# Optimization experiments

Hardware: AMD Instinct MI355X
Metric: run time of the kernel (lower is better)

## Reference

```python
import jax, jax.numpy as jnp
import numpy as np

D_MODEL, D_FF, N_EXP, TOP_K = 1024, 2048, 8, 2


def _silu(x):
    return x * jax.nn.sigmoid(x)


def setup_inputs() -> dict:
    key = jax.random.key(0)
    ks = jax.random.split(key, 8)
    s_d = 1.0 / np.sqrt(D_MODEL)
    s_f = 1.0 / np.sqrt(D_FF)
    x = jax.random.normal(ks[0], (2, 2048, D_MODEL), dtype=jnp.float32)
    Wr = jax.random.normal(ks[1], (D_MODEL, N_EXP), dtype=jnp.float32) * s_d
    W1 = jax.random.normal(ks[2], (N_EXP, D_MODEL, D_FF), dtype=jnp.float32) * s_d
    W2 = jax.random.normal(ks[3], (N_EXP, D_FF, D_MODEL), dtype=jnp.float32) * s_f
    W3 = jax.random.normal(ks[4], (N_EXP, D_MODEL, D_FF), dtype=jnp.float32) * s_d
    Ws1 = jax.random.normal(ks[5], (D_MODEL, D_FF), dtype=jnp.float32) * s_d
    Ws2 = jax.random.normal(ks[6], (D_FF, D_MODEL), dtype=jnp.float32) * s_f
    Ws3 = jax.random.normal(ks[7], (D_MODEL, D_FF), dtype=jnp.float32) * s_d
    return {"x": x, "Wr": Wr, "W1": W1, "W2": W2, "W3": W3,
            "Ws1": Ws1, "Ws2": Ws2, "Ws3": Ws3}


def reference(x, Wr, W1, W2, W3, Ws1, Ws2, Ws3):
    B, S, D = x.shape
    T = B * S
    # router
    logits = jnp.einsum('bsd,de->bse', x, Wr)                     # [B,S,E]
    z_loss = jnp.mean(jax.nn.logsumexp(logits, axis=-1) ** 2)
    router_probs = jax.nn.softmax(logits, axis=-1)
    topk_logits, topk_idx = jax.lax.top_k(logits, TOP_K)          # [B,S,K]
    topk_gates = jax.nn.softmax(topk_logits, axis=-1)             # top_k > 1 branch
    # load-balance loss
    p = jnp.mean(router_probs, axis=(0, 1))                       # [E]
    dispatch = jax.nn.one_hot(topk_idx, N_EXP, dtype=router_probs.dtype)  # [B,S,K,E]
    f = jnp.mean(dispatch, axis=(0, 1, 2))                        # [E]
    lb_loss = N_EXP * jnp.sum(p * f)
    # expert compute: run all experts densely, then gather routed outputs
    xf = x.reshape(T, D)
    h = _silu(jnp.einsum('td,edf->etf', xf, W1)) * jnp.einsum('td,edf->etf', xf, W3)
    y = jnp.einsum('etf,efd->etd', h, W2)                         # [E,T,D]
    yt = jnp.transpose(y, (1, 0, 2))                              # [T,E,D]
    idx_flat = topk_idx.reshape(T, TOP_K)
    gates_flat = topk_gates.reshape(T, TOP_K)
    sel = jnp.take_along_axis(yt, idx_flat[:, :, None], axis=1)   # [T,K,D]
    out_flat = jnp.sum(gates_flat[:, :, None] * sel, axis=1)      # [T,D]
    tokens_per_expert = jnp.sum(dispatch.reshape(-1, N_EXP), axis=0) / (T * TOP_K)
    # shared expert (applied sequentially; 1 shared expert here)
    out = out_flat.reshape(B, S, D)
    out = jnp.einsum('bsf,fd->bsd', _silu(jnp.einsum('bsd,df->bsf', out, Ws1)) * jnp.einsum('bsd,df->bsf', out, Ws3), Ws2)
    return (out, tokens_per_expert, z_loss, z_loss * 0.001, lb_loss, lb_loss * 0.1)
```

## Files before the change

### kernel.cpp

```cpp
#include <hip/hip_runtime.h>

#define TOKENS 4096
#define DM 1024
#define DFF 2048
#define NE 8
#define CAP 2048

typedef unsigned short u16;
typedef __attribute__((ext_vector_type(8))) __bf16 bf16x8;
typedef __attribute__((ext_vector_type(8))) unsigned short u16x8;
typedef __attribute__((ext_vector_type(4))) float f32x4;

#define GL16(g, l)                                                                        \
  __builtin_amdgcn_global_load_lds((const __attribute__((address_space(1))) void*)(g),    \
                                   (__attribute__((address_space(3))) void*)(l), 16, 0, 0)

__device__ __forceinline__ u16 f2bf(float f) {
  unsigned int u = __builtin_bit_cast(unsigned int, f);
  unsigned int r = (u + 0x7FFFu + ((u >> 16) & 1u)) >> 16;
  return (u16)r;
}
__device__ __forceinline__ float bf2f(u16 h) {
  unsigned int u = ((unsigned int)h) << 16;
  return __builtin_bit_cast(float, u);
}

__global__ void zero_k(int* counters) {
  if (threadIdx.x < NE) counters[threadIdx.x] = 0;
}

__global__ void conv_k(const float* __restrict__ src, u16* __restrict__ dst, int n4) {
  int i = blockIdx.x * 256 + threadIdx.x;
  if (i >= n4) return;
  float4 v = ((const float4*)src)[i];
  ushort4 ov = make_ushort4(f2bf(v.x), f2bf(v.y), f2bf(v.z), f2bf(v.w));
  ((ushort4*)dst)[i] = ov;
}

__global__ void tconv_k(const float* __restrict__ src, u16* __restrict__ dst, int K, int N) {
  __shared__ u16 tile[64][68];
  const int k0 = blockIdx.x * 64;
  const int n0 = blockIdx.y * 64;
  const size_t zoff = (size_t)blockIdx.z * K * N;
  const float* s = src + zoff;
  u16* d = dst + zoff;
  const int tid = threadIdx.x;
#pragma unroll
  for (int p = 0; p < 4; ++p) {
    int idx = p * 256 + tid;
    int kr = idx >> 4;
    int nc = (idx & 15) * 4;
    float4 v = *(const float4*)(s + (size_t)(k0 + kr) * N + (n0 + nc));
    tile[kr][nc + 0] = f2bf(v.x);
    tile[kr][nc + 1] = f2bf(v.y);
    tile[kr][nc + 2] = f2bf(v.z);
    tile[kr][nc + 3] = f2bf(v.w);
  }
  __syncthreads();
#pragma unroll
  for (int p = 0; p < 4; ++p) {
    int idx = p * 256 + tid;
    int nr = idx >> 4;
    int kc = (idx & 15) * 4;
    ushort4 ov = make_ushort4(tile[kc + 0][nr], tile[kc + 1][nr], tile[kc + 2][nr], tile[kc + 3][nr]);
    *(ushort4*)(d + (size_t)(n0 + nr) * K + (k0 + kc)) = ov;
  }
}

__global__ void router_k(const float* __restrict__ x, const float* __restrict__ Wr,
                         int* __restrict__ counters, int* __restrict__ tok_list,
                         int* __restrict__ tok_e, int* __restrict__ tok_slot,
                         float* __restrict__ tok_gate, float* __restrict__ tok_probs,
                         float* __restrict__ tok_lse) {
  const int t = blockIdx.x;
  const int l = threadIdx.x;
  float acc[NE];
#pragma unroll
  for (int e = 0; e < NE; ++e) acc[e] = 0.f;
  const float* xr = x + (size_t)t * DM;
#pragma unroll
  for (int it = 0; it < DM / 64; ++it) {
    int d = it * 64 + l;
    float xv = xr[d];
    const float4* wr = (const float4*)(Wr + (size_t)d * NE);
    float4 w0 = wr[0], w1 = wr[1];
    acc[0] += xv * w0.x; acc[1] += xv * w0.y; acc[2] += xv * w0.z; acc[3] += xv * w0.w;
    acc[4] += xv * w1.x; acc[5] += xv * w1.y; acc[6] += xv * w1.z; acc[7] += xv * w1.w;
  }
#pragma unroll
  for (int off = 32; off >= 1; off >>= 1) {
#pragma unroll
    for (int e = 0; e < NE; ++e) acc[e] += __shfl_xor(acc[e], off, 64);
  }
  if (l == 0) {
    float m = acc[0];
#pragma unroll
    for (int e = 1; e < NE; ++e) m = fmaxf(m, acc[e]);
    float ex[NE], s = 0.f;
#pragma unroll
    for (int e = 0; e < NE; ++e) { ex[e] = expf(acc[e] - m); s += ex[e]; }
    float inv = 1.f / s;
#pragma unroll
    for (int e = 0; e < NE; ++e) tok_probs[t * NE + e] = ex[e] * inv;
    tok_lse[t] = m + logf(s);
    int i0 = 0; float l0 = acc[0];
#pragma unroll
    for (int e = 1; e < NE; ++e) if (acc[e] > l0) { l0 = acc[e]; i0 = e; }
    int i1 = -1; float l1 = -3.0e38f;
#pragma unroll
    for (int e = 0; e < NE; ++e) if (e != i0 && acc[e] > l1) { l1 = acc[e]; i1 = e; }
    float e1 = expf(l1 - l0);
    float g0 = 1.f / (1.f + e1);
    float g1 = e1 / (1.f + e1);
    int p0 = atomicAdd(&counters[i0], 1);
    int p1 = atomicAdd(&counters[i1], 1);
    if (p0 < CAP) tok_list[i0 * CAP + p0] = t;
    if (p1 < CAP) tok_list[i1 * CAP + p1] = t;
    tok_e[t * 2 + 0] = i0; tok_e[t * 2 + 1] = i1;
    tok_slot[t * 2 + 0] = p0; tok_slot[t * 2 + 1] = p1;
    tok_gate[t * 2 + 0] = g0; tok_gate[t * 2 + 1] = g1;
  }
}

__global__ void finalize_k(const float* __restrict__ tok_probs, const float* __restrict__ tok_lse,
                           const int* __restrict__ counters, float* __restrict__ tail) {
  __shared__ float s_p[NE];
  __shared__ float s_z;
  const int tid = threadIdx.x;
  if (tid == 0) s_z = 0.f;
  if (tid < NE) s_p[tid] = 0.f;
  __syncthreads();
  float lp[NE] = {0, 0, 0, 0, 0, 0, 0, 0};
  float lz = 0.f;
  for (int t = tid; t < TOKENS; t += 256) {
    float l = tok_lse[t];
    lz += l * l;
#pragma unroll
    for (int e = 0; e < NE; ++e) lp[e] += tok_probs[t * NE + e];
  }
#pragma unroll
  for (int off = 32; off >= 1; off >>= 1) {
    lz += __shfl_xor(lz, off, 64);
#pragma unroll
    for (int e = 0; e < NE; ++e) lp[e] += __shfl_xor(lp[e], off, 64);
  }
  if ((tid & 63) == 0) {
    atomicAdd(&s_z, lz);
    for (int e = 0; e < NE; ++e) atomicAdd(&s_p[e], lp[e]);
  }
  __syncthreads();
  if (tid == 0) {
    float z = s_z / (float)TOKENS;
    float lb = 0.f;
    for (int e = 0; e < NE; ++e) {
      float f = (float)counters[e] / (float)(TOKENS * 2);
      float p = s_p[e] / (float)TOKENS;
      lb += p * f;
      tail[e] = f;
    }
    lb *= (float)NE;
    tail[8] = z;
    tail[9] = z * 0.001f;
    tail[10] = lb;
    tail[11] = lb * 0.1f;
  }
}

__launch_bounds__(256, 2)
__global__ void gemm1_k(const u16* __restrict__ A, const u16* __restrict__ B1g,
                        const u16* __restrict__ B3g, u16* __restrict__ Hout,
                        const int* __restrict__ tok_list, const int* __restrict__ counts,
                        int Mfix) {
  constexpr int K = DM;
  constexpr int N = DFF;
  const int e = blockIdx.z;
  int n_e = counts ? counts[e] : Mfix;
  if (counts && n_e > CAP) n_e = CAP;
  const int m_base = blockIdx.x * 128;
  if (m_base >= n_e) return;
  const int n_base = blockIdx.y * 128;
  const size_t bstride = counts ? (size_t)N * K : 0;
  const u16* B1 = B1g + (size_t)e * bstride;
  const u16* B3 = B3g + (size_t)e * bstride;

  __shared__ __align__(16) u16 Als[128 * 32];
  __shared__ __align__(16) u16 B1ls[128 * 32];
  __shared__ __align__(16) u16 B3ls[128 * 32];

  const int tid = threadIdx.x;
  const int lane = tid & 63;
  const int w = tid >> 6;
  const int wm = w >> 1, wn = w & 1;
  const int lo = lane & 15, hi = lane >> 4;

  const int c0 = 2 * w;
  const int r0 = c0 * 16 + (lane >> 2);
  const int r1 = r0 + 16;
  const int sg = lane & 3;

  size_t ar0, ar1;
  if (tok_list) {
    int g0i = m_base + r0; if (g0i >= n_e) g0i = n_e - 1;
    int g1i = m_base + r1; if (g1i >= n_e) g1i = n_e - 1;
    ar0 = (size_t)tok_list[e * CAP + g0i];
    ar1 = (size_t)tok_list[e * CAP + g1i];
  } else {
    ar0 = (size_t)(m_base + r0);
    ar1 = (size_t)(m_base + r1);
  }
  const u16* pA0 = A + ar0 * (size_t)K + sg * 8;
  const u16* pA1 = A + ar1 * (size_t)K + sg * 8;
  const u16* pB1a = B1 + (size_t)(n_base + r0) * K + sg * 8;
  const u16* pB1b = B1 + (size_t)(n_base + r1) * K + sg * 8;
  const u16* pB3a = B3 + (size_t)(n_base + r0) * K + sg * 8;
  const u16* pB3b = B3 + (size_t)(n_base + r1) * K + sg * 8;
  u16* lA0 = &Als[c0 * 512];  u16* lA1 = &Als[c0 * 512 + 512];
  u16* lB1a = &B1ls[c0 * 512]; u16* lB1b = &B1ls[c0 * 512 + 512];
  u16* lB3a = &B3ls[c0 * 512]; u16* lB3b = &B3ls[c0 * 512 + 512];

  f32x4 acc1[4][4], acc3[4][4];
#pragma unroll
  for (int i = 0; i < 4; ++i)
#pragma unroll
    for (int j = 0; j < 4; ++j) { acc1[i][j] = (f32x4)0.f; acc3[i][j] = (f32x4)0.f; }

  for (int kt = 0; kt < K / 32; ++kt) {
    __syncthreads();
    const int ko = kt * 32;
    GL16(pA0 + ko, lA0);
    GL16(pA1 + ko, lA1);
    GL16(pB1a + ko, lB1a);
    GL16(pB1b + ko, lB1b);
    GL16(pB3a + ko, lB3a);
    GL16(pB3b + ko, lB3b);
    __syncthreads();
    bf16x8 af[4], b1f[4], b3f[4];
#pragma unroll
    for (int i = 0; i < 4; ++i) {
      af[i] = *(const bf16x8*)&Als[(wm * 64 + i * 16 + lo) * 32 + hi * 8];
      b1f[i] = *(const bf16x8*)&B1ls[(wn * 64 + i * 16 + lo) * 32 + hi * 8];
      b3f[i] = *(const bf16x8*)&B3ls[(wn * 64 + i * 16 + lo) * 32 + hi * 8];
    }
#pragma unroll
    for (int i = 0; i < 4; ++i)
#pragma unroll
      for (int j = 0; j < 4; ++j) {
        acc1[i][j] = __builtin_amdgcn_mfma_f32_16x16x32_bf16(af[i], b1f[j], acc1[i][j], 0, 0, 0);
        acc3[i][j] = __builtin_amdgcn_mfma_f32_16x16x32_bf16(af[i], b3f[j], acc3[i][j], 0, 0, 0);
      }
  }

  const size_t orow0 = (counts ? (size_t)e * CAP : 0) + m_base;
#pragma unroll
  for (int i = 0; i < 4; ++i) {
#pragma unroll
    for (int r = 0; r < 4; ++r) {
      int rl = wm * 64 + i * 16 + hi * 4 + r;
      if (m_base + rl < n_e) {
        u16* orow = Hout + (orow0 + rl) * (size_t)N + n_base;
#pragma unroll
        for (int j = 0; j < 4; ++j) {
          float s1 = acc1[i][j][r], s3 = acc3[i][j][r];
          float hv = s1 / (1.f + __expf(-s1)) * s3;
          orow[wn * 64 + j * 16 + lo] = f2bf(hv);
        }
      }
    }
  }
}

__launch_bounds__(256, 2)
__global__ void gemm2_k(const u16* __restrict__ Ag, const u16* __restrict__ Bg,
                        void* __restrict__ Outv, const int* __restrict__ counts, int Mfix,
                        int outFloat) {
  constexpr int K = DFF;
  constexpr int N = DM;
  const int e = blockIdx.z;
  int n_e = counts ? counts[e] : Mfix;
  if (counts && n_e > CAP) n_e = CAP;
  const int m_base = blockIdx.x * 128;
  if (m_base >= n_e) return;
  const int n_base = blockIdx.y * 128;
  const u16* A = Ag + (counts ? (size_t)e * CAP * K : 0);
  const u16* B = Bg + (counts ? (size_t)e * N * K : 0);

  __shared__ __align__(16) u16 Als[128 * 32];
  __shared__ __align__(16) u16 Bls[128 * 32];

  const int tid = threadIdx.x;
  const int lane = tid & 63;
  const int w = tid >> 6;
  const int wm = w >> 1, wn = w & 1;
  const int lo = lane & 15, hi = lane >> 4;

  const int c0 = 2 * w;
  const int r0 = c0 * 16 + (lane >> 2);
  const int r1 = r0 + 16;
  const int sg = lane & 3;

  const u16* pA0 = A + (size_t)(m_base + r0) * K + sg * 8;
  const u16* pA1 = A + (size_t)(m_base + r1) * K + sg * 8;
  const u16* pB0 = B + (size_t)(n_base + r0) * K + sg * 8;
  const u16* pB1 = B + (size_t)(n_base + r1) * K + sg * 8;
  u16* lA0 = &Als[c0 * 512]; u16* lA1 = &Als[c0 * 512 + 512];
  u16* lB0 = &Bls[c0 * 512]; u16* lB1 = &Bls[c0 * 512 + 512];

  f32x4 acc[4][4];
#pragma unroll
  for (int i = 0; i < 4; ++i)
#pragma unroll
    for (int j = 0; j < 4; ++j) acc[i][j] = (f32x4)0.f;

  for (int kt = 0; kt < K / 32; ++kt) {
    __syncthreads();
    const int ko = kt * 32;
    GL16(pA0 + ko, lA0);
    GL16(pA1 + ko, lA1);
    GL16(pB0 + ko, lB0);
    GL16(pB1 + ko, lB1);
    __syncthreads();
    bf16x8 af[4], bfg[4];
#pragma unroll
    for (int i = 0; i < 4; ++i) {
      af[i] = *(const bf16x8*)&Als[(wm * 64 + i * 16 + lo) * 32 + hi * 8];
      bfg[i] = *(const bf16x8*)&Bls[(wn * 64 + i * 16 + lo) * 32 + hi * 8];
    }
#pragma unroll
    for (int i = 0; i < 4; ++i)
#pragma unroll
      for (int j = 0; j < 4; ++j)
        acc[i][j] = __builtin_amdgcn_mfma_f32_16x16x32_bf16(af[i], bfg[j], acc[i][j], 0, 0, 0);
  }

#pragma unroll
  for (int i = 0; i < 4; ++i) {
#pragma unroll
    for (int r = 0; r < 4; ++r) {
      int rl = wm * 64 + i * 16 + hi * 4 + r;
      if (m_base + rl < n_e) {
        if (outFloat) {
          float* orow = (float*)Outv + (size_t)(m_base + rl) * N + n_base;
#pragma unroll
          for (int j = 0; j < 4; ++j) orow[wn * 64 + j * 16 + lo] = acc[i][j][r];
        } else {
          u16* orow = (u16*)Outv + ((size_t)e * CAP + m_base + rl) * N + n_base;
#pragma unroll
          for (int j = 0; j < 4; ++j) orow[wn * 64 + j * 16 + lo] = f2bf(acc[i][j][r]);
        }
      }
    }
  }
}

__global__ void combine_k(const u16* __restrict__ Y, const int* __restrict__ tok_e,
                          const int* __restrict__ tok_slot, const float* __restrict__ tok_gate,
                          u16* __restrict__ xs) {
  int u = blockIdx.x * 256 + threadIdx.x;
  int t = u >> 7;
  int seg = (u & 127) * 8;
  int e0 = tok_e[t * 2 + 0], e1 = tok_e[t * 2 + 1];
  int s0 = tok_slot[t * 2 + 0], s1 = tok_slot[t * 2 + 1];
  float g0 = tok_gate[t * 2 + 0], g1 = tok_gate[t * 2 + 1];
  u16x8 y0 = *(const u16x8*)(Y + ((size_t)e0 * CAP + s0) * DM + seg);
  u16x8 y1 = *(const u16x8*)(Y + ((size_t)e1 * CAP + s1) * DM + seg);
  u16x8 o;
#pragma unroll
  for (int j = 0; j < 8; ++j) o[j] = f2bf(g0 * bf2f(y0[j]) + g1 * bf2f(y1[j]));
  *(u16x8*)(xs + (size_t)t * DM + seg) = o;
}

extern "C" void kernel_launch(void* const* d_in, const int* in_sizes, int n_in, void* d_out,
                              int out_size, void* d_ws, size_t ws_size, hipStream_t stream) {
  const float* x = (const float*)d_in[0];
  const float* Wr = (const float*)d_in[1];
  const float* W1 = (const float*)d_in[2];
  const float* W2 = (const float*)d_in[3];
  const float* W3 = (const float*)d_in[4];
  const float* Ws1 = (const float*)d_in[5];
  const float* Ws2 = (const float*)d_in[6];
  const float* Ws3 = (const float*)d_in[7];
  float* out = (float*)d_out;
  (void)in_sizes; (void)n_in; (void)out_size; (void)ws_size;

  char* ws = (char*)d_ws;
  size_t o = 0;
  auto alloc = [&](size_t b) {
    void* p = ws + o;
    o = (o + b + 255) & ~(size_t)255;
    return p;
  };
  int* counters = (int*)alloc(NE * 4);
  int* tok_e = (int*)alloc(TOKENS * 2 * 4);
  int* tok_slot = (int*)alloc(TOKENS * 2 * 4);
  float* tok_gate = (float*)alloc(TOKENS * 2 * 4);
  float* tok_probs = (float*)alloc(TOKENS * NE * 4);
  float* tok_lse = (float*)alloc(TOKENS * 4);
  int* tok_list = (int*)alloc(NE * CAP * 4);
  u16* xb = (u16*)alloc((size_t)TOKENS * DM * 2);
  u16* W1t = (u16*)alloc((size_t)NE * DFF * DM * 2);
  u16* W3t = (u16*)alloc((size_t)NE * DFF * DM * 2);
  u16* W2t = (u16*)alloc((size_t)NE * DM * DFF * 2);
  u16* Ws1t = (u16*)alloc((size_t)DFF * DM * 2);
  u16* Ws3t = (u16*)alloc((size_t)DFF * DM * 2);
  u16* Ws2t = (u16*)alloc((size_t)DM * DFF * 2);
  u16* H = (u16*)alloc((size_t)NE * CAP * DFF * 2);
  u16* Y = (u16*)alloc((size_t)NE * CAP * DM * 2);
  u16* xs = (u16*)alloc((size_t)TOKENS * DM * 2);
  u16* Hs = (u16*)alloc((size_t)TOKENS * DFF * 2);

  zero_k<<<1, 64, 0, stream>>>(counters);
  conv_k<<<TOKENS * DM / 4 / 256, 256, 0, stream>>>(x, xb, TOKENS * DM / 4);
  tconv_k<<<dim3(DM / 64, DFF / 64, NE), 256, 0, stream>>>(W1, W1t, DM, DFF);
  tconv_k<<<dim3(DM / 64, DFF / 64, NE), 256, 0, stream>>>(W3, W3t, DM, DFF);
  tconv_k<<<dim3(DFF / 64, DM / 64, NE), 256, 0, stream>>>(W2, W2t, DFF, DM);
  tconv_k<<<dim3(DM / 64, DFF / 64, 1), 256, 0, stream>>>(Ws1, Ws1t, DM, DFF);
  tconv_k<<<dim3(DM / 64, DFF / 64, 1), 256, 0, stream>>>(Ws3, Ws3t, DM, DFF);
  tconv_k<<<dim3(DFF / 64, DM / 64, 1), 256, 0, stream>>>(Ws2, Ws2t, DFF, DM);
  router_k<<<TOKENS, 64, 0, stream>>>(x, Wr, counters, tok_list, tok_e, tok_slot, tok_gate,
                                      tok_probs, tok_lse);
  finalize_k<<<1, 256, 0, stream>>>(tok_probs, tok_lse, counters, out + (size_t)TOKENS * DM);
  gemm1_k<<<dim3(CAP / 128, DFF / 128, NE), 256, 0, stream>>>(xb, W1t, W3t, H, tok_list,
                                                              counters, 0);
  gemm2_k<<<dim3(CAP / 128, DM / 128, NE), 256, 0, stream>>>(H, W2t, (void*)Y, counters, 0, 0);
  combine_k<<<TOKENS * DM / 8 / 256, 256, 0, stream>>>(Y, tok_e, tok_slot, tok_gate, xs);
  gemm1_k<<<dim3(TOKENS / 128, DFF / 128, 1), 256, 0, stream>>>(xs, Ws1t, Ws3t, Hs, nullptr,
                                                                nullptr, TOKENS);
  gemm2_k<<<dim3(TOKENS / 128, DM / 128, 1), 256, 0, stream>>>(Hs, Ws2t, (void*)out, nullptr,
                                                               TOKENS, 1);
}
```

Before: 705.6 us.

## Double-buffer LDS tiles in GEMMs and remap workgroups for XCD locality

Both GEMM kernels now use two LDS buffers so the global-to-LDS load of the next K tile is issued before the MFMA work on the current tile, removing one barrier per iteration. The grid is flattened to 1D, and block indices are remapped so consecutive logical tiles land on the same XCD (stride by 8), which is meant to improve L2 reuse of the weight and activation tiles. Double buffering doubles LDS use per block (48KB for gemm1), which may limit occupancy at 2 blocks per CU.

```diff
diff --git a/kernel.cpp b/kernel.cpp
--- a/kernel.cpp
+++ b/kernel.cpp
@@ -170,22 +170,30 @@
 __global__ void gemm1_k(const u16* __restrict__ A, const u16* __restrict__ B1g,
                         const u16* __restrict__ B3g, u16* __restrict__ Hout,
                         const int* __restrict__ tok_list, const int* __restrict__ counts,
-                        int Mfix) {
+                        int Mfix, int MBg, int NBg) {
   constexpr int K = DM;
   constexpr int N = DFF;
-  const int e = blockIdx.z;
+  constexpr int NT = K / 32;
+  const int nwg = gridDim.x;
+  const int cpx = nwg >> 3;
+  const int wg = (blockIdx.x & 7) * cpx + (blockIdx.x >> 3);
+  const int per = MBg * NBg;
+  const int e = wg / per;
+  const int rem = wg - e * per;
+  const int m_blk = rem % MBg;
+  const int n_blk = rem / MBg;
   int n_e = counts ? counts[e] : Mfix;
   if (counts && n_e > CAP) n_e = CAP;
-  const int m_base = blockIdx.x * 128;
+  const int m_base = m_blk * 128;
   if (m_base >= n_e) return;
-  const int n_base = blockIdx.y * 128;
+  const int n_base = n_blk * 128;
   const size_t bstride = counts ? (size_t)N * K : 0;
   const u16* B1 = B1g + (size_t)e * bstride;
   const u16* B3 = B3g + (size_t)e * bstride;
 
-  __shared__ __align__(16) u16 Als[128 * 32];
-  __shared__ __align__(16) u16 B1ls[128 * 32];
-  __shared__ __align__(16) u16 B3ls[128 * 32];
+  __shared__ __align__(16) u16 Als[2][128 * 32];
+  __shared__ __align__(16) u16 B1ls[2][128 * 32];
+  __shared__ __align__(16) u16 B3ls[2][128 * 32];
 
   const int tid = threadIdx.x;
   const int lane = tid & 63;
@@ -214,9 +222,6 @@
   const u16* pB1b = B1 + (size_t)(n_base + r1) * K + sg * 8;
   const u16* pB3a = B3 + (size_t)(n_base + r0) * K + sg * 8;
   const u16* pB3b = B3 + (size_t)(n_base + r1) * K + sg * 8;
-  u16* lA0 = &Als[c0 * 512];  u16* lA1 = &Als[c0 * 512 + 512];
-  u16* lB1a = &B1ls[c0 * 512]; u16* lB1b = &B1ls[c0 * 512 + 512];
-  u16* lB3a = &B3ls[c0 * 512]; u16* lB3b = &B3ls[c0 * 512 + 512];
 
   f32x4 acc1[4][4], acc3[4][4];
 #pragma unroll
@@ -224,22 +229,13 @@
 #pragma unroll
     for (int j = 0; j < 4; ++j) { acc1[i][j] = (f32x4)0.f; acc3[i][j] = (f32x4)0.f; }
 
-  for (int kt = 0; kt < K / 32; ++kt) {
-    __syncthreads();
-    const int ko = kt * 32;
-    GL16(pA0 + ko, lA0);
-    GL16(pA1 + ko, lA1);
-    GL16(pB1a + ko, lB1a);
-    GL16(pB1b + ko, lB1b);
-    GL16(pB3a + ko, lB3a);
-    GL16(pB3b + ko, lB3b);
-    __syncthreads();
+  auto compute = [&](const u16* rA, const u16* rB1, const u16* rB3) {
     bf16x8 af[4], b1f[4], b3f[4];
 #pragma unroll
     for (int i = 0; i < 4; ++i) {
-      af[i] = *(const bf16x8*)&Als[(wm * 64 + i * 16 + lo) * 32 + hi * 8];
-      b1f[i] = *(const bf16x8*)&B1ls[(wn * 64 + i * 16 + lo) * 32 + hi * 8];
-      b3f[i] = *(const bf16x8*)&B3ls[(wn * 64 + i * 16 + lo) * 32 + hi * 8];
+      af[i] = *(const bf16x8*)&rA[(wm * 64 + i * 16 + lo) * 32 + hi * 8];
+      b1f[i] = *(const bf16x8*)&rB1[(wn * 64 + i * 16 + lo) * 32 + hi * 8];
+      b3f[i] = *(const bf16x8*)&rB3[(wn * 64 + i * 16 + lo) * 32 + hi * 8];
     }
 #pragma unroll
     for (int i = 0; i < 4; ++i)
@@ -248,7 +244,30 @@
         acc1[i][j] = __builtin_amdgcn_mfma_f32_16x16x32_bf16(af[i], b1f[j], acc1[i][j], 0, 0, 0);
         acc3[i][j] = __builtin_amdgcn_mfma_f32_16x16x32_bf16(af[i], b3f[j], acc3[i][j], 0, 0, 0);
       }
-  }
+  };
+
+  GL16(pA0, &Als[0][c0 * 512]);  GL16(pA1, &Als[0][c0 * 512 + 512]);
+  GL16(pB1a, &B1ls[0][c0 * 512]); GL16(pB1b, &B1ls[0][c0 * 512 + 512]);
+  GL16(pB3a, &B3ls[0][c0 * 512]); GL16(pB3b, &B3ls[0][c0 * 512 + 512]);
+  __syncthreads();
+  int cur = 0;
+  for (int kt = 0; kt < NT - 1; ++kt) {
+    const int ko = (kt + 1) * 32;
+    u16* sA = cur ? &Als[0][c0 * 512] : &Als[1][c0 * 512];
+    u16* sB1 = cur ? &B1ls[0][c0 * 512] : &B1ls[1][c0 * 512];
+    u16* sB3 = cur ? &B3ls[0][c0 * 512] : &B3ls[1][c0 * 512];
+    GL16(pA0 + ko, sA);  GL16(pA1 + ko, sA + 512);
+    GL16(pB1a + ko, sB1); GL16(pB1b + ko, sB1 + 512);
+    GL16(pB3a + ko, sB3); GL16(pB3b + ko, sB3 + 512);
+    compute(cur ? &Als[1][0] : &Als[0][0],
+            cur ? &B1ls[1][0] : &B1ls[0][0],
+            cur ? &B3ls[1][0] : &B3ls[0][0]);
+    __syncthreads();
+    cur ^= 1;
+  }
+  compute(cur ? &Als[1][0] : &Als[0][0],
+          cur ? &B1ls[1][0] : &B1ls[0][0],
+          cur ? &B3ls[1][0] : &B3ls[0][0]);
 
   const size_t orow0 = (counts ? (size_t)e * CAP : 0) + m_base;
 #pragma unroll
@@ -272,20 +291,28 @@
 __launch_bounds__(256, 2)
 __global__ void gemm2_k(const u16* __restrict__ Ag, const u16* __restrict__ Bg,
                         void* __restrict__ Outv, const int* __restrict__ counts, int Mfix,
-                        int outFloat) {
+                        int outFloat, int MBg, int NBg) {
   constexpr int K = DFF;
   constexpr int N = DM;
-  const int e = blockIdx.z;
+  constexpr int NT = K / 32;
+  const int nwg = gridDim.x;
+  const int cpx = nwg >> 3;
+  const int wg = (blockIdx.x & 7) * cpx + (blockIdx.x >> 3);
+  const int per = MBg * NBg;
+  const int e = wg / per;
+  const int rem = wg - e * per;
+  const int m_blk = rem % MBg;
+  const int n_blk = rem / MBg;
   int n_e = counts ? counts[e] : Mfix;
   if (counts && n_e > CAP) n_e = CAP;
-  const int m_base = blockIdx.x * 128;
+  const int m_base = m_blk * 128;
   if (m_base >= n_e) return;
-  const int n_base = blockIdx.y * 128;
+  const int n_base = n_blk * 128;
   const u16* A = Ag + (counts ? (size_t)e * CAP * K : 0);
   const u16* B = Bg + (counts ? (size_t)e * N * K : 0);
 
-  __shared__ __align__(16) u16 Als[128 * 32];
-  __shared__ __align__(16) u16 Bls[128 * 32];
+  __shared__ __align__(16) u16 Als[2][128 * 32];
+  __shared__ __align__(16) u16 Bls[2][128 * 32];
 
   const int tid = threadIdx.x;
   const int lane = tid & 63;
@@ -302,8 +329,6 @@
   const u16* pA1 = A + (size_t)(m_base + r1) * K + sg * 8;
   const u16* pB0 = B + (size_t)(n_base + r0) * K + sg * 8;
   const u16* pB1 = B + (size_t)(n_base + r1) * K + sg * 8;
-  u16* lA0 = &Als[c0 * 512]; u16* lA1 = &Als[c0 * 512 + 512];
-  u16* lB0 = &Bls[c0 * 512]; u16* lB1 = &Bls[c0 * 512 + 512];
 
   f32x4 acc[4][4];
 #pragma unroll
@@ -311,26 +336,35 @@
 #pragma unroll
     for (int j = 0; j < 4; ++j) acc[i][j] = (f32x4)0.f;
 
-  for (int kt = 0; kt < K / 32; ++kt) {
-    __syncthreads();
-    const int ko = kt * 32;
-    GL16(pA0 + ko, lA0);
-    GL16(pA1 + ko, lA1);
-    GL16(pB0 + ko, lB0);
-    GL16(pB1 + ko, lB1);
-    __syncthreads();
+  auto compute = [&](const u16* rA, const u16* rB) {
     bf16x8 af[4], bfg[4];
 #pragma unroll
     for (int i = 0; i < 4; ++i) {
-      af[i] = *(const bf16x8*)&Als[(wm * 64 + i * 16 + lo) * 32 + hi * 8];
-      bfg[i] = *(const bf16x8*)&Bls[(wn * 64 + i * 16 + lo) * 32 + hi * 8];
+      af[i] = *(const bf16x8*)&rA[(wm * 64 + i * 16 + lo) * 32 + hi * 8];
+      bfg[i] = *(const bf16x8*)&rB[(wn * 64 + i * 16 + lo) * 32 + hi * 8];
     }
 #pragma unroll
     for (int i = 0; i < 4; ++i)
 #pragma unroll
       for (int j = 0; j < 4; ++j)
         acc[i][j] = __builtin_amdgcn_mfma_f32_16x16x32_bf16(af[i], bfg[j], acc[i][j], 0, 0, 0);
-  }
+  };
+
+  GL16(pA0, &Als[0][c0 * 512]); GL16(pA1, &Als[0][c0 * 512 + 512]);
+  GL16(pB0, &Bls[0][c0 * 512]); GL16(pB1, &Bls[0][c0 * 512 + 512]);
+  __syncthreads();
+  int cur = 0;
+  for (int kt = 0; kt < NT - 1; ++kt) {
+    const int ko = (kt + 1) * 32;
+    u16* sA = cur ? &Als[0][c0 * 512] : &Als[1][c0 * 512];
+    u16* sB = cur ? &Bls[0][c0 * 512] : &Bls[1][c0 * 512];
+    GL16(pA0 + ko, sA); GL16(pA1 + ko, sA + 512);
+    GL16(pB0 + ko, sB); GL16(pB1 + ko, sB + 512);
+    compute(cur ? &Als[1][0] : &Als[0][0], cur ? &Bls[1][0] : &Bls[0][0]);
+    __syncthreads();
+    cur ^= 1;
+  }
+  compute(cur ? &Als[1][0] : &Als[0][0], cur ? &Bls[1][0] : &Bls[0][0]);
 
 #pragma unroll
   for (int i = 0; i < 4; ++i) {
@@ -419,12 +453,9 @@
   router_k<<<TOKENS, 64, 0, stream>>>(x, Wr, counters, tok_list, tok_e, tok_slot, tok_gate,
                                       tok_probs, tok_lse);
   finalize_k<<<1, 256, 0, stream>>>(tok_probs, tok_lse, counters, out + (size_t)TOKENS * DM);
-  gemm1_k<<<dim3(CAP / 128, DFF / 128, NE), 256, 0, stream>>>(xb, W1t, W3t, H, tok_list,
-                                                              counters, 0);
-  gemm2_k<<<dim3(CAP / 128, DM / 128, NE), 256, 0, stream>>>(H, W2t, (void*)Y, counters, 0, 0);
+  gemm1_k<<<16 * 16 * NE, 256, 0, stream>>>(xb, W1t, W3t, H, tok_list, counters, 0, 16, 16);
+  gemm2_k<<<16 * 8 * NE, 256, 0, stream>>>(H, W2t, (void*)Y, counters, 0, 0, 16, 8);
   combine_k<<<TOKENS * DM / 8 / 256, 256, 0, stream>>>(Y, tok_e, tok_slot, tok_gate, xs);
-  gemm1_k<<<dim3(TOKENS / 128, DFF / 128, 1), 256, 0, stream>>>(xs, Ws1t, Ws3t, Hs, nullptr,
-                                                                nullptr, TOKENS);
-  gemm2_k<<<dim3(TOKENS / 128, DM / 128, 1), 256, 0, stream>>>(Hs, Ws2t, (void*)out, nullptr,
-                                                               TOKENS, 1);
-}
+  gemm1_k<<<32 * 16, 256, 0, stream>>>(xs, Ws1t, Ws3t, Hs, nullptr, nullptr, TOKENS, 32, 16);
+  gemm2_k<<<32 * 8, 256, 0, stream>>>(Hs, Ws2t, (void*)out, nullptr, TOKENS, 1, 32, 8);
+}
```

Result: faster. 617.6 us (-12.5%).
